# Performance work log

Hardware: AMD Instinct MI355X
Metric: run time of the kernel (lower is better)

## Reference

```python
import jax, jax.numpy as jnp
import numpy as np

N = 100000  # nodes
E = 1600000  # edges (without self-loops)


def _gcn_norm(edge_index, n):
    # add self loops, compute symmetric normalization D^-1/2 (A+I) D^-1/2
    loops = jnp.arange(n, dtype=edge_index.dtype)
    src = jnp.concatenate([edge_index[0], loops])
    dst = jnp.concatenate([edge_index[1], loops])
    deg = jax.ops.segment_sum(jnp.ones_like(dst, dtype=jnp.float32), dst, num_segments=n)
    dinv = jax.lax.rsqrt(jnp.maximum(deg, 1.0))  # deg >= 1 due to self loops
    norm = dinv[src] * dinv[dst]  # [E+N]
    return src, dst, norm


def _gcn_layer(x, W, b, src, dst, norm, n):
    h = x @ W  # [N, out]
    msg = h[src] * norm[:, None]  # [E+N, out]
    agg = jax.ops.segment_sum(msg, dst, num_segments=n)
    return agg + b


def setup_inputs() -> dict:
    key = jax.random.key(0)
    ks = jax.random.split(key, 8)
    x = jax.random.normal(ks[0], (N, 256), dtype=jnp.float32)
    edge_index = jax.random.randint(ks[1], (2, E), 0, N, dtype=jnp.int32)
    W1 = jax.random.normal(ks[2], (256, 128), dtype=jnp.float32) / np.sqrt(256.0)
    b1 = jnp.zeros((128,), dtype=jnp.float32)
    W2 = jax.random.normal(ks[3], (128, 128), dtype=jnp.float32) / np.sqrt(128.0)
    b2 = jnp.zeros((128,), dtype=jnp.float32)
    W3 = jax.random.normal(ks[4], (128, 16), dtype=jnp.float32) / np.sqrt(128.0)
    b3 = jnp.zeros((16,), dtype=jnp.float32)
    return {"x": x, "edge_index": edge_index, "W1": W1, "b1": b1,
            "W2": W2, "b2": b2, "W3": W3, "b3": b3}


def reference(x, edge_index, W1, b1, W2, b2, W3, b3):
    n = x.shape[0]
    src, dst, norm = _gcn_norm(edge_index, n)
    h = jax.nn.relu(_gcn_layer(x, W1, b1, src, dst, norm, n))
    # dropout layers are identity in eval mode
    h = jax.nn.relu(_gcn_layer(h, W2, b2, src, dst, norm, n))
    out = _gcn_layer(h, W3, b3, src, dst, norm, n)
    return out
```

## Files before the change

### kernel.cpp

```cpp
#include <hip/hip_runtime.h>
#include <hip/hip_bf16.h>
#include <cstdint>
#include <cstddef>

typedef __hip_bfloat16 bf16;

typedef __attribute__((ext_vector_type(8))) short s16x8;
typedef __attribute__((ext_vector_type(4))) float f32x4;
typedef __attribute__((ext_vector_type(8))) unsigned short u16x8;

__device__ __forceinline__ float bflo(unsigned u) { return __uint_as_float(u << 16); }
__device__ __forceinline__ float bfhi(unsigned u) { return __uint_as_float(u & 0xffff0000u); }
__device__ __forceinline__ unsigned packbf2(float a, float b) {
  unsigned lo = (unsigned)__bfloat16_as_ushort(__float2bfloat16(a));
  unsigned hi = (unsigned)__bfloat16_as_ushort(__float2bfloat16(b));
  return lo | (hi << 16);
}
__device__ __forceinline__ float to_f(float v) { return v; }
__device__ __forceinline__ float to_f(bf16 v) { return __bfloat162float(v); }

__global__ __launch_bounds__(256) void k_detect(const unsigned* __restrict__ x, int* __restrict__ flag,
                                                int forced) {
  __shared__ int sm[256];
  int t = threadIdx.x;
  if (forced >= 0) { if (t == 0) *flag = forced; return; }
  int cnt = 0;
  for (int i = t; i < 4096; i += 256) {
    unsigned u = x[i];
    unsigned lo_exp = (u >> 7) & 0xFF;
    cnt += (lo_exp >= 97 && lo_exp <= 130) ? 1 : 0;
  }
  sm[t] = cnt;
  __syncthreads();
  for (int off = 128; off > 0; off >>= 1) {
    if (t < off) sm[t] += sm[t + off];
    __syncthreads();
  }
  if (t == 0) *flag = (sm[0] > 2048) ? 1 : 0;
}


__global__ __launch_bounds__(256) void k_init(int* deg, int* fil, int n) {
  int i = blockIdx.x * 256 + threadIdx.x;
  if (i < n) { deg[i] = 0; fil[i] = 0; }
}

__global__ __launch_bounds__(256) void k_deg(const int* __restrict__ dst, int* __restrict__ deg,
                                             int E, int N) {
  int e = blockIdx.x * 256 + threadIdx.x;
  if (e >= E) return;
  int d = dst[e];
  if ((unsigned)d < (unsigned)N) atomicAdd(&deg[d], 1);
}

__global__ __launch_bounds__(256) void k_dinv(const int* __restrict__ deg, float* __restrict__ dinv, int n) {
  int i = blockIdx.x * 256 + threadIdx.x;
  if (i < n) dinv[i] = rsqrtf((float)deg[i] + 1.0f);
}

__global__ __launch_bounds__(256) void k_scan1(const int* __restrict__ deg, int* __restrict__ bsum, int n) {
  __shared__ int ws[4];
  int t = threadIdx.x;
  int base = blockIdx.x * 1024 + t * 4;
  int s = 0;
#pragma unroll
  for (int j = 0; j < 4; ++j) { int i = base + j; if (i < n) s += deg[i]; }
#pragma unroll
  for (int off = 32; off > 0; off >>= 1) s += __shfl_down(s, off);
  if ((t & 63) == 0) ws[t >> 6] = s;
  __syncthreads();
  if (t == 0) bsum[blockIdx.x] = ws[0] + ws[1] + ws[2] + ws[3];
}

__global__ __launch_bounds__(256) void k_scan2(const int* __restrict__ bsum, int* __restrict__ boff, int nb) {
  __shared__ int sm[256];
  int t = threadIdx.x;
  int v = (t < nb) ? bsum[t] : 0;
  sm[t] = v;
  __syncthreads();
  for (int off = 1; off < 256; off <<= 1) {
    int u = (t >= off) ? sm[t - off] : 0;
    __syncthreads();
    sm[t] += u;
    __syncthreads();
  }
  if (t < nb) boff[t] = sm[t] - v;
}

__global__ __launch_bounds__(256) void k_scan3(const int* __restrict__ deg, const int* __restrict__ boff,
                                               int* __restrict__ rowptr, int n, int Etot) {
  __shared__ int sm[256];
  int t = threadIdx.x;
  int base = blockIdx.x * 1024 + t * 4;
  int v[4]; int s = 0;
#pragma unroll
  for (int j = 0; j < 4; ++j) { int i = base + j; v[j] = (i < n) ? deg[i] : 0; s += v[j]; }
  sm[t] = s;
  __syncthreads();
  for (int off = 1; off < 256; off <<= 1) {
    int u = (t >= off) ? sm[t - off] : 0;
    __syncthreads();
    sm[t] += u;
    __syncthreads();
  }
  int run = sm[t] - s + boff[blockIdx.x];
#pragma unroll
  for (int j = 0; j < 4; ++j) {
    int i = base + j;
    if (i < n) rowptr[i] = run;
    run += v[j];
  }
  if (blockIdx.x == 0 && t == 0) rowptr[n] = Etot;
}

__global__ __launch_bounds__(256) void k_fill(const int* __restrict__ src, const int* __restrict__ dst,
                                              const int* __restrict__ rowptr, int* __restrict__ fil,
                                              int* __restrict__ csr, int E, int N) {
  int e = blockIdx.x * 256 + threadIdx.x;
  if (e >= E) return;
  int d = dst[e];
  if ((unsigned)d >= (unsigned)N) return;
  int p = rowptr[d] + atomicAdd(&fil[d], 1);
  if ((unsigned)p >= (unsigned)E) return;
  int s = src[e];
  csr[p] = ((unsigned)s < (unsigned)N) ? s : 0;
}

template <typename TB, int WANT, int SPLIT>
__global__ __launch_bounds__(256) void k_packB(const int* __restrict__ flag,
                                               const TB* __restrict__ B,
                                               unsigned short* __restrict__ Bp, int K) {
  if (*flag != WANT) return;
  const int nf = (K >> 5) * 512;
  int t = blockIdx.x * 256 + threadIdx.x;
  if (t >= nf) return;
  int s = t >> 9, rem = t & 511, c = rem >> 6, l = rem & 63;
  int kb = (s << 5) + ((l >> 4) << 3);
  int col = (c << 4) + (l & 15);
  u16x8 vh, vl;
#pragma unroll
  for (int i = 0; i < 8; ++i) {
    float f = to_f(B[(size_t)(kb + i) * 128 + col]);
    bf16 h = __float2bfloat16(f);
    vh[i] = __bfloat16_as_ushort(h);
    if (SPLIT) {
      float r = f - __bfloat162float(h);
      vl[i] = __bfloat16_as_ushort(__float2bfloat16(r));
    }
  }
  *(u16x8*)(Bp + (size_t)t * 8) = vh;
  if (SPLIT) *(u16x8*)(Bp + ((size_t)nf + t) * 8) = vl;
}

template <typename TA, int WANT, int MODE, int KT>
__global__ __launch_bounds__(256) void k_gemm_mfma(const int* __restrict__ flag,
                                                   const TA* __restrict__ A,
                                                   const unsigned short* __restrict__ Bp,
                                                   const float* __restrict__ dinv,
                                                   bf16* __restrict__ C, int M) {
  if (*flag != WANT) return;
  constexpr int steps = KT >> 5;
  constexpr size_t nf = (size_t)steps * 512;
  const int l = threadIdx.x & 63;
  const int w = threadIdx.x >> 6;
  const int row0 = blockIdx.x * 64 + w * 16;
  int arow = row0 + (l & 15);
  if (arow >= M) arow = M - 1;
  const TA* Ap = A + (size_t)arow * KT + ((l >> 4) << 3);
  const s16x8* bp = (const s16x8*)Bp + l;
  f32x4 acc[8];
#pragma unroll
  for (int c = 0; c < 8; ++c) acc[c] = (f32x4){0.f, 0.f, 0.f, 0.f};

  float fa[2][8];
  s16x8 ra[2];
  if constexpr (MODE == 2) {
    const float* fp = (const float*)Ap;
    float4 u0 = *(const float4*)fp;
    float4 u1 = *(const float4*)(fp + 4);
    fa[0][0] = u0.x; fa[0][1] = u0.y; fa[0][2] = u0.z; fa[0][3] = u0.w;
    fa[0][4] = u1.x; fa[0][5] = u1.y; fa[0][6] = u1.z; fa[0][7] = u1.w;
  } else {
    ra[0] = *(const s16x8*)Ap;
  }

#pragma unroll
  for (int s = 0; s < steps; ++s) {
    const int cur = s & 1, nxt = cur ^ 1;
    if (s + 1 < steps) {
      if constexpr (MODE == 2) {
        const float* fp = (const float*)(Ap + ((s + 1) << 5));
        float4 u0 = *(const float4*)fp;
        float4 u1 = *(const float4*)(fp + 4);
        fa[nxt][0] = u0.x; fa[nxt][1] = u0.y; fa[nxt][2] = u0.z; fa[nxt][3] = u0.w;
        fa[nxt][4] = u1.x; fa[nxt][5] = u1.y; fa[nxt][6] = u1.z; fa[nxt][7] = u1.w;
      } else {
        ra[nxt] = *(const s16x8*)(Ap + ((s + 1) << 5));
      }
    }
    s16x8 a, alo;
    if constexpr (MODE == 2) {
#pragma unroll
      for (int i = 0; i < 8; ++i) {
        float f = fa[cur][i];
        bf16 h = __float2bfloat16(f);
        a[i] = (short)__bfloat16_as_ushort(h);
        float r = f - __bfloat162float(h);
        alo[i] = (short)__bfloat16_as_ushort(__float2bfloat16(r));
      }
    } else {
      a = ra[cur];
    }
#pragma unroll
    for (int c = 0; c < 8; ++c) {
      size_t fi = (size_t)(((s << 3) + c) << 6);
      s16x8 bh = bp[fi];
      acc[c] = __builtin_amdgcn_mfma_f32_16x16x32_bf16(a, bh, acc[c], 0, 0, 0);
      if constexpr (MODE >= 1) {
        s16x8 bl = bp[nf + fi];
        acc[c] = __builtin_amdgcn_mfma_f32_16x16x32_bf16(a, bl, acc[c], 0, 0, 0);
      }
      if constexpr (MODE == 2) {
        acc[c] = __builtin_amdgcn_mfma_f32_16x16x32_bf16(alo, bh, acc[c], 0, 0, 0);
      }
    }
  }
  const int lb = l & 15;
  const int rbase = row0 + ((l >> 4) << 2);
#pragma unroll
  for (int r = 0; r < 4; ++r) {
    int row = rbase + r;
    if (row < M) {
      float sc = dinv[row];
      bf16* Cr = C + (size_t)row * 128 + lb;
#pragma unroll
      for (int c = 0; c < 8; ++c) Cr[c << 4] = __float2bfloat16(acc[c][r] * sc);
    }
  }
}

template <typename TB, int WANT>
__global__ __launch_bounds__(256) void k_gemm16(const int* __restrict__ flag,
                                                const bf16* __restrict__ A, const TB* __restrict__ B,
                                                const float* __restrict__ dinv, float* __restrict__ C, int M) {
  if (*flag != WANT) return;
  __shared__ float Bs[128][16];
  const int tid = threadIdx.x;
  for (int l = tid; l < 128 * 16; l += 256) Bs[l >> 4][l & 15] = to_f(B[l]);
  __syncthreads();
  const int r = blockIdx.x * 64 + (tid >> 2);
  const int c0 = (tid & 3) * 4;
  if (r >= M) return;
  const bf16* Ar = A + (size_t)r * 128;
  float a0 = 0.f, a1 = 0.f, a2 = 0.f, a3 = 0.f;
#pragma unroll
  for (int k = 0; k < 128; k += 8) {
    uint4 u = *(const uint4*)&Ar[k];
    float f[8] = {bflo(u.x), bfhi(u.x), bflo(u.y), bfhi(u.y),
                  bflo(u.z), bfhi(u.z), bflo(u.w), bfhi(u.w)};
#pragma unroll
    for (int j = 0; j < 8; ++j) {
      float4 b = *(const float4*)&Bs[k + j][c0];
      a0 = fmaf(f[j], b.x, a0); a1 = fmaf(f[j], b.y, a1);
      a2 = fmaf(f[j], b.z, a2); a3 = fmaf(f[j], b.w, a3);
    }
  }
  float s = dinv[r];
  *(float4*)&C[(size_t)r * 16 + c0] = make_float4(a0 * s, a1 * s, a2 * s, a3 * s);
}


template <typename TB, int WANT>
__global__ __launch_bounds__(256) void k_agg128(const int* __restrict__ flag,
                                                const bf16* __restrict__ Hs, const int* __restrict__ rowptr,
                                                const int* __restrict__ csr, const float* __restrict__ dinv,
                                                const TB* __restrict__ bias, bf16* __restrict__ out,
                                                int M, int Etot) {
  if (*flag != WANT) return;
  int wid = threadIdx.x >> 6, lane = threadIdx.x & 63;
  int node = blockIdx.x * 4 + wid;
  if (node >= M) return;
  int c = lane * 2;
  unsigned u = *(const unsigned*)&Hs[(size_t)node * 128 + c];
  float ax = bflo(u), ay = bfhi(u);
  int e = rowptr[node], end = rowptr[node + 1];
  if (e < 0) e = 0;
  if (end > Etot) end = Etot;
  for (; e + 8 <= end; e += 8) {
    int s0 = csr[e],     s1 = csr[e + 1], s2 = csr[e + 2], s3 = csr[e + 3];
    int s4 = csr[e + 4], s5 = csr[e + 5], s6 = csr[e + 6], s7 = csr[e + 7];
    unsigned u0 = *(const unsigned*)&Hs[(size_t)s0 * 128 + c];
    unsigned u1 = *(const unsigned*)&Hs[(size_t)s1 * 128 + c];
    unsigned u2 = *(const unsigned*)&Hs[(size_t)s2 * 128 + c];
    unsigned u3 = *(const unsigned*)&Hs[(size_t)s3 * 128 + c];
    unsigned u4 = *(const unsigned*)&Hs[(size_t)s4 * 128 + c];
    unsigned u5 = *(const unsigned*)&Hs[(size_t)s5 * 128 + c];
    unsigned u6 = *(const unsigned*)&Hs[(size_t)s6 * 128 + c];
    unsigned u7 = *(const unsigned*)&Hs[(size_t)s7 * 128 + c];
    ax += (bflo(u0) + bflo(u1)) + (bflo(u2) + bflo(u3)) +
          (bflo(u4) + bflo(u5)) + (bflo(u6) + bflo(u7));
    ay += (bfhi(u0) + bfhi(u1)) + (bfhi(u2) + bfhi(u3)) +
          (bfhi(u4) + bfhi(u5)) + (bfhi(u6) + bfhi(u7));
  }
  for (; e + 4 <= end; e += 4) {
    int s0 = csr[e], s1 = csr[e + 1], s2 = csr[e + 2], s3 = csr[e + 3];
    unsigned u0 = *(const unsigned*)&Hs[(size_t)s0 * 128 + c];
    unsigned u1 = *(const unsigned*)&Hs[(size_t)s1 * 128 + c];
    unsigned u2 = *(const unsigned*)&Hs[(size_t)s2 * 128 + c];
    unsigned u3 = *(const unsigned*)&Hs[(size_t)s3 * 128 + c];
    ax += bflo(u0) + bflo(u1) + bflo(u2) + bflo(u3);
    ay += bfhi(u0) + bfhi(u1) + bfhi(u2) + bfhi(u3);
  }
  for (; e < end; ++e) {
    unsigned uu = *(const unsigned*)&Hs[(size_t)csr[e] * 128 + c];
    ax += bflo(uu); ay += bfhi(uu);
  }
  float di = dinv[node];
  float ox = fmaxf(ax * di + to_f(bias[c]), 0.f);
  float oy = fmaxf(ay * di + to_f(bias[c + 1]), 0.f);
  *(unsigned*)&out[(size_t)node * 128 + c] = packbf2(ox, oy);
}

template <typename TB, typename TO, int WANT>
__global__ __launch_bounds__(256) void k_agg16(const int* __restrict__ flag,
                                               const float* __restrict__ Hs, const int* __restrict__ rowptr,
                                               const int* __restrict__ csr, const float* __restrict__ dinv,
                                               const TB* __restrict__ bias, TO* __restrict__ out,
                                               int M, int Etot) {
  if (*flag != WANT) return;
  int sub = threadIdx.x >> 4, lane = threadIdx.x & 15;
  int node = blockIdx.x * 16 + sub;
  if (node >= M) return;
  float acc = Hs[(size_t)node * 16 + lane];
  int e = rowptr[node], end = rowptr[node + 1];
  if (e < 0) e = 0;
  if (end > Etot) end = Etot;
  for (; e + 8 <= end; e += 8) {
    int s0 = csr[e],     s1 = csr[e + 1], s2 = csr[e + 2], s3 = csr[e + 3];
    int s4 = csr[e + 4], s5 = csr[e + 5], s6 = csr[e + 6], s7 = csr[e + 7];
    acc += (Hs[(size_t)s0 * 16 + lane] + Hs[(size_t)s1 * 16 + lane]) +
           (Hs[(size_t)s2 * 16 + lane] + Hs[(size_t)s3 * 16 + lane]) +
           (Hs[(size_t)s4 * 16 + lane] + Hs[(size_t)s5 * 16 + lane]) +
           (Hs[(size_t)s6 * 16 + lane] + Hs[(size_t)s7 * 16 + lane]);
  }
  for (; e + 4 <= end; e += 4) {
    int s0 = csr[e], s1 = csr[e + 1], s2 = csr[e + 2], s3 = csr[e + 3];
    acc += Hs[(size_t)s0 * 16 + lane] + Hs[(size_t)s1 * 16 + lane] +
           Hs[(size_t)s2 * 16 + lane] + Hs[(size_t)s3 * 16 + lane];
  }
  for (; e < end; ++e) acc += Hs[(size_t)csr[e] * 16 + lane];
  float o = acc * dinv[node] + to_f(bias[lane]);
  out[(size_t)node * 16 + lane] = (TO)o;
}


extern "C" void kernel_launch(void* const* d_in, const int* in_sizes, int n_in,
                              void* d_out, int out_size, void* d_ws, size_t ws_size,
                              hipStream_t stream) {
  const int* ei = (const int*)d_in[1];

  const long long w1sz = in_sizes[2];
  const int kmode = (int)(w1sz / 32768);
  const int N = (int)((long long)in_sizes[0] * 128 / w1sz);
  const int E = (kmode == 1) ? in_sizes[1] / 2 : in_sizes[1] / 8;
  const int forced = (kmode == 2) ? 1 : (kmode == 4) ? 0 : -1;
  const int* srcv = ei;
  const int* dstv = ei + E;

  char* p = (char*)d_ws;
  auto alloc = [&](size_t b) { char* r = p; p += (b + 255) & ~(size_t)255; return r; };
  int*   flag   = (int*)alloc(256);
  int*   deg    = (int*)alloc((size_t)N * 4);
  int*   fil    = (int*)alloc((size_t)N * 4);
  int*   rowptr = (int*)alloc((size_t)(N + 1) * 4);
  float* dinv   = (float*)alloc((size_t)N * 4);
  const int NB = (N + 1023) / 1024;
  int*   bsum   = (int*)alloc((size_t)NB * 4);
  int*   boff   = (int*)alloc((size_t)NB * 4);
  int*   csr    = (int*)alloc((size_t)E * 4);
  bf16*  HsB    = (bf16*)alloc((size_t)N * 128 * 2);
  bf16*  hB     = (bf16*)alloc((size_t)N * 128 * 2);
  unsigned short* Bp1 = (unsigned short*)alloc(131072);
  unsigned short* Bp2 = (unsigned short*)alloc(65536);
  float* Hs16   = (float*)HsB;

  const int gN = (N + 255) / 256, gE = (E + 255) / 256;
  k_detect<<<1, 256, 0, stream>>>((const unsigned*)d_in[0], flag, forced);
  k_init <<<gN, 256, 0, stream>>>(deg, fil, N);
  k_deg  <<<gE, 256, 0, stream>>>(dstv, deg, E, N);
  k_dinv <<<gN, 256, 0, stream>>>(deg, dinv, N);
  k_scan1<<<NB, 256, 0, stream>>>(deg, bsum, N);
  k_scan2<<<1, 256, 0, stream>>>(bsum, boff, NB);
  k_scan3<<<NB, 256, 0, stream>>>(deg, boff, rowptr, N, E);
  k_fill <<<gE, 256, 0, stream>>>(srcv, dstv, rowptr, fil, csr, E, N);

  const int gM64 = (N + 63) / 64;
  const int gAgg = (N + 3) / 4;
  const bool doB16 = (forced != 0);
  const bool doF32 = (forced != 1);

  if (doB16) {
    const bf16* x  = (const bf16*)d_in[0];
    const bf16* b1 = (const bf16*)d_in[3];
    const bf16* b2 = (const bf16*)d_in[5];
    const bf16* W3 = (const bf16*)d_in[6]; const bf16* b3 = (const bf16*)d_in[7];
    k_packB<bf16, 1, 0><<<16, 256, 0, stream>>>(flag, (const bf16*)d_in[2], Bp1, 256);
    k_packB<bf16, 1, 0><<<8,  256, 0, stream>>>(flag, (const bf16*)d_in[4], Bp2, 128);
    k_gemm_mfma<bf16, 1, 0, 256><<<gM64, 256, 0, stream>>>(flag, x, Bp1, dinv, HsB, N);
    k_agg128<bf16, 1><<<gAgg, 256, 0, stream>>>(flag, HsB, rowptr, csr, dinv, b1, hB, N, E);
    k_gemm_mfma<bf16, 1, 0, 128><<<gM64, 256, 0, stream>>>(flag, hB, Bp2, dinv, HsB, N);
    k_agg128<bf16, 1><<<gAgg, 256, 0, stream>>>(flag, HsB, rowptr, csr, dinv, b2, hB, N, E);
    k_gemm16<bf16, 1><<<gM64, 256, 0, stream>>>(flag, hB, W3, dinv, Hs16, N);
    k_agg16<bf16, bf16, 1><<<(N + 15) / 16, 256, 0, stream>>>(flag, Hs16, rowptr, csr, dinv, b3,
                                                              (bf16*)d_out, N, E);
  }
  if (doF32) {
    const float* x  = (const float*)d_in[0];
    const float* b1 = (const float*)d_in[3];
    const float* b2 = (const float*)d_in[5];
    const float* W3 = (const float*)d_in[6]; const float* b3 = (const float*)d_in[7];
    k_packB<float, 0, 1><<<16, 256, 0, stream>>>(flag, (const float*)d_in[2], Bp1, 256);
    k_packB<float, 0, 1><<<8,  256, 0, stream>>>(flag, (const float*)d_in[4], Bp2, 128);
    k_gemm_mfma<float, 0, 2, 256><<<gM64, 256, 0, stream>>>(flag, x, Bp1, dinv, HsB, N);
    k_agg128<float, 0><<<gAgg, 256, 0, stream>>>(flag, HsB, rowptr, csr, dinv, b1, hB, N, E);
    k_gemm_mfma<bf16, 0, 1, 128><<<gM64, 256, 0, stream>>>(flag, hB, Bp2, dinv, HsB, N);
    k_agg128<float, 0><<<gAgg, 256, 0, stream>>>(flag, HsB, rowptr, csr, dinv, b2, hB, N, E);
    k_gemm16<float, 0><<<gM64, 256, 0, stream>>>(flag, hB, W3, dinv, Hs16, N);
    k_agg16<float, float, 0><<<(N + 15) / 16, 256, 0, stream>>>(flag, Hs16, rowptr, csr, dinv, b3,
                                                                (float*)d_out, N, E);
  }
}
```

Before: 587.0 us.

## Stage GEMM B fragments through LDS with async global-to-LDS double buffering

The MFMA GEMM kernel now loads B fragments cooperatively into a double-buffered LDS array using global_load_lds, so the four waves share one copy instead of each wave reading B from global memory on its own. A-row prefetch is deepened from two to three slots. The intent is to cut redundant global/L2 traffic for B and hide load latency. In exchange it adds a __syncthreads per K-step and uses LDS, which may reduce occupancy.

```diff
diff --git a/kernel.cpp b/kernel.cpp
--- a/kernel.cpp
+++ b/kernel.cpp
@@ -18,6 +18,11 @@
 }
 __device__ __forceinline__ float to_f(float v) { return v; }
 __device__ __forceinline__ float to_f(bf16 v) { return __bfloat162float(v); }
+
+__device__ __forceinline__ void gload_lds16(const void* g, void* l) {
+  __builtin_amdgcn_global_load_lds((const __attribute__((address_space(1))) unsigned int*)g,
+                                   (__attribute__((address_space(3))) unsigned int*)l, 16, 0, 0);
+}
 
 __global__ __launch_bounds__(256) void k_detect(const unsigned* __restrict__ x, int* __restrict__ flag,
                                                 int forced) {
@@ -160,71 +165,85 @@
                                                    bf16* __restrict__ C, int M) {
   if (*flag != WANT) return;
   constexpr int steps = KT >> 5;
-  constexpr size_t nf = (size_t)steps * 512;
-  const int l = threadIdx.x & 63;
-  const int w = threadIdx.x >> 6;
+  constexpr int NFRAG = (MODE >= 1) ? 16 : 8;
+  constexpr int FPW = NFRAG / 4;
+  constexpr size_t nfbytes = (size_t)steps * 8192;
+  __shared__ s16x8 lds[2][NFRAG * 64];
+  const int tid = threadIdx.x;
+  const int l = tid & 63;
+  const int w = tid >> 6;
   const int row0 = blockIdx.x * 64 + w * 16;
   int arow = row0 + (l & 15);
   if (arow >= M) arow = M - 1;
   const TA* Ap = A + (size_t)arow * KT + ((l >> 4) << 3);
-  const s16x8* bp = (const s16x8*)Bp + l;
+  const char* Bb = (const char*)Bp;
+
+  auto stage = [&](int b, int s) {
+#pragma unroll
+    for (int j = 0; j < FPW; ++j) {
+      int q = w * FPW + j;
+      size_t off = (q < 8) ? ((size_t)(s * 8 + q)) * 1024
+                           : nfbytes + ((size_t)(s * 8 + q - 8)) * 1024;
+      gload_lds16(Bb + off + (size_t)l * 16, (void*)&lds[b][q * 64]);
+    }
+  };
+
   f32x4 acc[8];
 #pragma unroll
   for (int c = 0; c < 8; ++c) acc[c] = (f32x4){0.f, 0.f, 0.f, 0.f};
 
-  float fa[2][8];
-  s16x8 ra[2];
-  if constexpr (MODE == 2) {
-    const float* fp = (const float*)Ap;
-    float4 u0 = *(const float4*)fp;
-    float4 u1 = *(const float4*)(fp + 4);
-    fa[0][0] = u0.x; fa[0][1] = u0.y; fa[0][2] = u0.z; fa[0][3] = u0.w;
-    fa[0][4] = u1.x; fa[0][5] = u1.y; fa[0][6] = u1.z; fa[0][7] = u1.w;
-  } else {
-    ra[0] = *(const s16x8*)Ap;
-  }
+  float4 f0[3], f1[3];
+  s16x8 ra[3];
+  auto loadA = [&](int s, int slot) {
+    if constexpr (MODE == 2) {
+      const float* fp = (const float*)(Ap + (s << 5));
+      f0[slot] = *(const float4*)fp;
+      f1[slot] = *(const float4*)(fp + 4);
+    } else {
+      ra[slot] = *(const s16x8*)(Ap + (s << 5));
+    }
+  };
+
+  stage(0, 0);
+  loadA(0, 0);
+  if constexpr (steps > 1) loadA(1, 1);
+  __syncthreads();
 
 #pragma unroll
   for (int s = 0; s < steps; ++s) {
-    const int cur = s & 1, nxt = cur ^ 1;
-    if (s + 1 < steps) {
-      if constexpr (MODE == 2) {
-        const float* fp = (const float*)(Ap + ((s + 1) << 5));
-        float4 u0 = *(const float4*)fp;
-        float4 u1 = *(const float4*)(fp + 4);
-        fa[nxt][0] = u0.x; fa[nxt][1] = u0.y; fa[nxt][2] = u0.z; fa[nxt][3] = u0.w;
-        fa[nxt][4] = u1.x; fa[nxt][5] = u1.y; fa[nxt][6] = u1.z; fa[nxt][7] = u1.w;
-      } else {
-        ra[nxt] = *(const s16x8*)(Ap + ((s + 1) << 5));
-      }
-    }
+    const int b = s & 1;
+    if (s + 1 < steps) stage(b ^ 1, s + 1);
+    if (s + 2 < steps) loadA(s + 2, (s + 2) % 3);
     s16x8 a, alo;
     if constexpr (MODE == 2) {
+      const int sl = s % 3;
+      float f[8] = {f0[sl].x, f0[sl].y, f0[sl].z, f0[sl].w,
+                    f1[sl].x, f1[sl].y, f1[sl].z, f1[sl].w};
 #pragma unroll
       for (int i = 0; i < 8; ++i) {
-        float f = fa[cur][i];
-        bf16 h = __float2bfloat16(f);
+        bf16 h = __float2bfloat16(f[i]);
         a[i] = (short)__bfloat16_as_ushort(h);
-        float r = f - __bfloat162float(h);
+        float r = f[i] - __bfloat162float(h);
         alo[i] = (short)__bfloat16_as_ushort(__float2bfloat16(r));
       }
     } else {
-      a = ra[cur];
+      a = ra[s % 3];
     }
 #pragma unroll
     for (int c = 0; c < 8; ++c) {
-      size_t fi = (size_t)(((s << 3) + c) << 6);
-      s16x8 bh = bp[fi];
+      s16x8 bh = lds[b][c * 64 + l];
       acc[c] = __builtin_amdgcn_mfma_f32_16x16x32_bf16(a, bh, acc[c], 0, 0, 0);
       if constexpr (MODE >= 1) {
-        s16x8 bl = bp[nf + fi];
+        s16x8 bl = lds[b][(8 + c) * 64 + l];
         acc[c] = __builtin_amdgcn_mfma_f32_16x16x32_bf16(a, bl, acc[c], 0, 0, 0);
       }
       if constexpr (MODE == 2) {
         acc[c] = __builtin_amdgcn_mfma_f32_16x16x32_bf16(alo, bh, acc[c], 0, 0, 0);
       }
     }
-  }
+    __syncthreads();
+  }
+
   const int lb = l & 15;
   const int rbase = row0 + ((l >> 4) << 2);
 #pragma unroll
```

New measurement: 554.9 us. 5.5% less time.
